# Optimization experiments

Hardware: AMD Instinct MI355X
Metric: run time of the kernel (lower is better)

## Reference

```python
import jax, jax.numpy as jnp
import numpy as np

B, T, D_MODEL, D_HIDDEN, MAX_SEQLEN = 4, 2048, 1024, 256, 2048


def setup_inputs() -> dict:
    key = jax.random.key(0)
    ks = jax.random.split(key, 8)
    s_in = 1.0 / np.sqrt(D_MODEL)
    s_out = 1.0 / np.sqrt(D_HIDDEN)
    # xavier_uniform bound for W_bias (fan_in = fan_out = MAX_SEQLEN)
    xb = np.sqrt(6.0 / (MAX_SEQLEN + MAX_SEQLEN))
    return {
        "q": jax.random.normal(ks[0], (B, T, D_MODEL), jnp.float32),
        "k": jax.random.normal(ks[1], (B, T, D_MODEL), jnp.float32),
        "v": jax.random.normal(ks[2], (B, T, D_MODEL), jnp.float32),
        "Wq": jax.random.normal(ks[3], (D_MODEL, D_HIDDEN), jnp.float32) * s_in,
        "Wk": jax.random.normal(ks[4], (D_MODEL, D_HIDDEN), jnp.float32) * s_in,
        "Wv": jax.random.normal(ks[5], (D_MODEL, D_HIDDEN), jnp.float32) * s_in,
        "Wo": jax.random.normal(ks[6], (D_HIDDEN, D_MODEL), jnp.float32) * s_out,
        "W_bias": jax.random.uniform(ks[7], (MAX_SEQLEN, MAX_SEQLEN), jnp.float32, -xb, xb),
    }


def reference(q, k, v, Wq, Wk, Wv, Wo, W_bias):
    Ti, Tj = q.shape[1], k.shape[1]
    Q = q @ Wq                      # [B,Ti,dh]
    K = k @ Wk                      # [B,Tj,dh]
    V = v @ Wv                      # [B,Tj,dh]
    pos_bias = W_bias[:Ti, :Tj][None]               # [1,Ti,Tj]
    # NOTE: source subtracts max over dim 0 (batch). For pos_bias that dim is 1,
    # so exp_pos_bias == exp(0) == ones -- reproduced faithfully here.
    max_key = jnp.max(K, axis=0, keepdims=True)      # [1,Tj,dh]
    max_pos_bias = jnp.max(pos_bias, axis=0, keepdims=True)
    exp_key = jnp.exp(K - max_key)                   # [B,Tj,dh]
    exp_pos_bias = jnp.exp(pos_bias - max_pos_bias)  # [1,Ti,Tj]
    num = jnp.einsum('ij,bjd->bid', exp_pos_bias[0], exp_key * V)  # [B,Ti,dh]
    den = jnp.einsum('ij,bjd->bid', exp_pos_bias[0], exp_key)      # [B,Ti,dh]
    Yt = jax.nn.sigmoid(Q) * num / den
    return Yt @ Wo                  # [B,Ti,d_model]
```

## Files before the change

kernel.cpp:

```cpp
#include <hip/hip_runtime.h>
#include <hip/hip_bf16.h>
#include <math.h>

#define B_   4
#define T_   2048
#define DM   1024
#define DH   256
#define M_   (B_*T_)

typedef __bf16 bf16;
typedef __attribute__((ext_vector_type(8))) __bf16 bf16x8;
typedef __attribute__((ext_vector_type(4))) float  f32x4;

__device__ inline float sigmoidf_(float x) { return 1.0f / (1.0f + __expf(-x)); }

__device__ inline int swz8(int r, int c) { return (((c >> 3) ^ (r & 7)) << 3); }

__global__ void transpose_cvt_all(const float* __restrict__ Wq, const float* __restrict__ Wk,
                                  const float* __restrict__ Wv, const float* __restrict__ Wo,
                                  bf16* __restrict__ Wq_t, bf16* __restrict__ Wk_t,
                                  bf16* __restrict__ Wv_t, bf16* __restrict__ Wo_t)
{
    const int bid = blockIdx.x;
    __shared__ float tile[32][33];
    const int w = bid >> 8, t = bid & 255;
    const float* in; bf16* out; int R, C, sh;
    if      (w == 0) { in = Wq; out = Wq_t; R = DM; C = DH; sh = 3; }
    else if (w == 1) { in = Wk; out = Wk_t; R = DM; C = DH; sh = 3; }
    else if (w == 2) { in = Wv; out = Wv_t; R = DM; C = DH; sh = 3; }
    else             { in = Wo; out = Wo_t; R = DH; C = DM; sh = 5; }
    const int r0 = (t >> sh) * 32, c0 = (t & ((1 << sh) - 1)) * 32;
    const int tx = threadIdx.x & 31, ty = threadIdx.x >> 5;
    #pragma unroll
    for (int i = ty; i < 32; i += 8)
        tile[i][tx] = in[(long)(r0 + i) * C + c0 + tx];
    __syncthreads();
    #pragma unroll
    for (int i = ty; i < 32; i += 8)
        out[(long)(c0 + i) * R + r0 + tx] = (bf16)tile[tx][i];
}

__global__ __launch_bounds__(512, 6)
void gemm_proj(const float* __restrict__ qin, const float* __restrict__ kin,
               const float* __restrict__ vin,
               const bf16* __restrict__ Wq_t, const bf16* __restrict__ Wk_t,
               const bf16* __restrict__ Wv_t,
               bf16* __restrict__ Yb, bf16* __restrict__ Kb, bf16* __restrict__ Vb)
{
    __shared__ __align__(16) bf16 As[2][64][64];
    __shared__ __align__(16) bf16 Bs[2][128][64];

    const int z = blockIdx.z;
    const float* A  = (z == 0) ? qin  : (z == 1) ? kin  : vin;
    const bf16*  Wt = (z == 0) ? Wq_t : (z == 1) ? Wk_t : Wv_t;
    bf16*        C  = (z == 0) ? Yb   : (z == 1) ? Kb   : Vb;

    const int bid  = blockIdx.x;
    const int tile = (bid & 7) * 32 + (bid >> 3);
    const int m0 = (tile >> 1) * 64;
    const int n0 = (tile & 1) * 128;

    const int tid = threadIdx.x, lane = tid & 63, wave = tid >> 6;
    const int wr = wave >> 2, wc = wave & 3;
    const int q4 = lane >> 4, l16 = lane & 15;

    f32x4 acc[2][2] = {};
    const int ar = tid >> 3, ac8 = (tid & 7) * 8;
    const int br = tid >> 2, bc16 = (tid & 3) * 16;

    const float* aBase = &A[(long)(m0 + ar) * DM + ac8];
    const bf16*  bBase = &Wt[(long)(n0 + br) * DM + bc16];

    f32x4  pa0[2], pa1[2];
    bf16x8 pb0[2], pb1[2];
    #pragma unroll
    for (int p = 0; p < 2; ++p) {
        const float* ap = aBase + p * 64;
        pa0[p] = *(const f32x4*)ap; pa1[p] = *(const f32x4*)(ap + 4);
        const bf16* bp = bBase + p * 64;
        pb0[p] = *(const bf16x8*)bp; pb1[p] = *(const bf16x8*)(bp + 8);
    }
    {
        bf16x8 o;
        #pragma unroll
        for (int e = 0; e < 4; ++e) { o[e] = (bf16)pa0[0][e]; o[4 + e] = (bf16)pa1[0][e]; }
        *(bf16x8*)&As[0][ar][swz8(ar, ac8)]      = o;
        *(bf16x8*)&Bs[0][br][swz8(br, bc16)]     = pb0[0];
        *(bf16x8*)&Bs[0][br][swz8(br, bc16 + 8)] = pb1[0];
    }
    __syncthreads();

    #pragma unroll
    for (int s = 0; s < 16; ++s) {
        const int cs = s & 1;
        const int ns = cs ^ 1;
        if (s + 2 < 16) {
            const float* ap = aBase + (s + 2) * 64;
            pa0[cs] = *(const f32x4*)ap; pa1[cs] = *(const f32x4*)(ap + 4);
            const bf16* bp = bBase + (s + 2) * 64;
            pb0[cs] = *(const bf16x8*)bp; pb1[cs] = *(const bf16x8*)(bp + 8);
        }
        if (s + 1 < 16) {
            bf16x8 o;
            #pragma unroll
            for (int e = 0; e < 4; ++e) { o[e] = (bf16)pa0[ns][e]; o[4 + e] = (bf16)pa1[ns][e]; }
            *(bf16x8*)&As[ns][ar][swz8(ar, ac8)]      = o;
            *(bf16x8*)&Bs[ns][br][swz8(br, bc16)]     = pb0[ns];
            *(bf16x8*)&Bs[ns][br][swz8(br, bc16 + 8)] = pb1[ns];
        }
        #pragma unroll
        for (int kk = 0; kk < 64; kk += 32) {
            const int ra = wr * 32 + l16, rb = wc * 32 + l16;
            bf16x8 a0 = *(const bf16x8*)&As[cs][ra     ][swz8(ra,      kk + q4 * 8)];
            bf16x8 a1 = *(const bf16x8*)&As[cs][ra + 16][swz8(ra + 16, kk + q4 * 8)];
            bf16x8 b0 = *(const bf16x8*)&Bs[cs][rb     ][swz8(rb,      kk + q4 * 8)];
            bf16x8 b1 = *(const bf16x8*)&Bs[cs][rb + 16][swz8(rb + 16, kk + q4 * 8)];
            acc[0][0] = __builtin_amdgcn_mfma_f32_16x16x32_bf16(a0, b0, acc[0][0], 0, 0, 0);
            acc[0][1] = __builtin_amdgcn_mfma_f32_16x16x32_bf16(a0, b1, acc[0][1], 0, 0, 0);
            acc[1][0] = __builtin_amdgcn_mfma_f32_16x16x32_bf16(a1, b0, acc[1][0], 0, 0, 0);
            acc[1][1] = __builtin_amdgcn_mfma_f32_16x16x32_bf16(a1, b1, acc[1][1], 0, 0, 0);
        }
        __syncthreads();
    }
    #pragma unroll
    for (int i = 0; i < 2; ++i)
        #pragma unroll
        for (int j = 0; j < 2; ++j)
            #pragma unroll
            for (int r = 0; r < 4; ++r) {
                int gm = m0 + wr * 32 + i * 16 + q4 * 4 + r;
                int gn = n0 + wc * 32 + j * 16 + l16;
                float v = acc[i][j][r];
                C[(long)gm * DH + gn] = (bf16)((z == 0) ? sigmoidf_(v) : v);
            }
}

__global__ void reduce_kv(const bf16* __restrict__ Kb, const bf16* __restrict__ Vb,
                          float* __restrict__ part)
{
    __shared__ float red[2][4][B_][DH];
    const int tid = threadIdx.x;
    const int g = tid & 31, jj = tid >> 5;
    const int d8 = g * 8;

    float sn[B_][8] = {}, sd[B_][8] = {};
    #pragma unroll
    for (int t2 = 0; t2 < 2; ++t2) {
        const int j = blockIdx.x * 16 + t2 * 8 + jj;
        bf16x8 kx[B_], vx[B_];
        #pragma unroll
        for (int b = 0; b < B_; ++b) {
            kx[b] = *(const bf16x8*)&Kb[((long)b * T_ + j) * DH + d8];
            vx[b] = *(const bf16x8*)&Vb[((long)b * T_ + j) * DH + d8];
        }
        #pragma unroll
        for (int e = 0; e < 8; ++e) {
            float k0 = (float)kx[0][e], k1 = (float)kx[1][e];
            float k2 = (float)kx[2][e], k3 = (float)kx[3][e];
            float mx = fmaxf(fmaxf(k0, k1), fmaxf(k2, k3));
            float e0 = __expf(k0 - mx), e1 = __expf(k1 - mx);
            float e2 = __expf(k2 - mx), e3 = __expf(k3 - mx);
            sn[0][e] += e0 * (float)vx[0][e]; sd[0][e] += e0;
            sn[1][e] += e1 * (float)vx[1][e]; sd[1][e] += e1;
            sn[2][e] += e2 * (float)vx[2][e]; sd[2][e] += e2;
            sn[3][e] += e3 * (float)vx[3][e]; sd[3][e] += e3;
        }
    }
    #pragma unroll
    for (int b = 0; b < B_; ++b)
        #pragma unroll
        for (int e = 0; e < 8; ++e) {
            sn[b][e] += __shfl_xor(sn[b][e], 32);
            sd[b][e] += __shfl_xor(sd[b][e], 32);
        }
    const int w = tid >> 6;
    if ((tid & 32) == 0) {
        #pragma unroll
        for (int b = 0; b < B_; ++b)
            #pragma unroll
            for (int e = 0; e < 8; ++e) {
                red[0][w][b][d8 + e] = sn[b][e];
                red[1][w][b][d8 + e] = sd[b][e];
            }
    }
    __syncthreads();
    float* pout = &part[(long)blockIdx.x * 2048];
    #pragma unroll
    for (int o = tid; o < 2 * B_ * DH; o += 256) {
        const int arr = o >> 10, b = (o >> 8) & 3, d = o & 255;
        pout[o] = red[arr][0][b][d] + red[arr][1][b][d]
                + red[arr][2][b][d] + red[arr][3][b][d];
    }
}

__global__ void merge_kv(const float* __restrict__ part, float* __restrict__ rv)
{
    const int t = blockIdx.x * 256 + threadIdx.x;
    float num = 0.f, den = 0.f;
    for (int blk = 0; blk < 128; ++blk) {
        num += part[(long)blk * 2048 + t];
        den += part[(long)blk * 2048 + 1024 + t];
    }
    rv[t] = num / den;
}

__global__ __launch_bounds__(512, 6)
void gemm_out(const bf16* __restrict__ Yb, const bf16* __restrict__ Wo_t,
              const float* __restrict__ rv, float* __restrict__ out)
{
    __shared__ __align__(16) bf16 As[2][64][64];
    __shared__ __align__(16) bf16 Bs[2][128][64];
    __shared__ float rv_s[DH];

    const int bid  = blockIdx.x;
    const int tile = (bid & 7) * 128 + (bid >> 3);
    const int m0 = (tile >> 3) * 64;
    const int n0 = (tile & 7) * 128;
    const int b  = m0 >> 11;

    const int tid = threadIdx.x, lane = tid & 63, wave = tid >> 6;
    const int wr = wave >> 2, wc = wave & 3;
    const int q4 = lane >> 4, l16 = lane & 15;

    if (tid < DH) rv_s[tid] = rv[b * DH + tid];

    f32x4 acc[2][2] = {};
    const int ar = tid >> 3, ac8 = (tid & 7) * 8;
    const int br = tid >> 2, bc16 = (tid & 3) * 16;

    const bf16* aBase = &Yb[(long)(m0 + ar) * DH + ac8];
    const bf16* bBase = &Wo_t[(long)(n0 + br) * DH + bc16];

    bf16x8 pq[2], pb0[2], pb1[2];
    #pragma unroll
    for (int p = 0; p < 2; ++p) {
        pq[p]  = *(const bf16x8*)(aBase + p * 64);
        const bf16* wp = bBase + p * 64;
        pb0[p] = *(const bf16x8*)wp; pb1[p] = *(const bf16x8*)(wp + 8);
    }
    __syncthreads();
    {
        bf16x8 o;
        #pragma unroll
        for (int e = 0; e < 8; ++e)
            o[e] = (bf16)((float)pq[0][e] * rv_s[ac8 + e]);
        *(bf16x8*)&As[0][ar][swz8(ar, ac8)]      = o;
        *(bf16x8*)&Bs[0][br][swz8(br, bc16)]     = pb0[0];
        *(bf16x8*)&Bs[0][br][swz8(br, bc16 + 8)] = pb1[0];
    }
    __syncthreads();

    #pragma unroll
    for (int s = 0; s < 4; ++s) {
        const int cs = s & 1, ns = cs ^ 1;
        if (s + 2 < 4) {
            pq[cs]  = *(const bf16x8*)(aBase + (s + 2) * 64);
            const bf16* wp = bBase + (s + 2) * 64;
            pb0[cs] = *(const bf16x8*)wp; pb1[cs] = *(const bf16x8*)(wp + 8);
        }
        if (s + 1 < 4) {
            bf16x8 o;
            #pragma unroll
            for (int e = 0; e < 8; ++e)
                o[e] = (bf16)((float)pq[ns][e] * rv_s[(s + 1) * 64 + ac8 + e]);
            *(bf16x8*)&As[ns][ar][swz8(ar, ac8)]      = o;
            *(bf16x8*)&Bs[ns][br][swz8(br, bc16)]     = pb0[ns];
            *(bf16x8*)&Bs[ns][br][swz8(br, bc16 + 8)] = pb1[ns];
        }
        #pragma unroll
        for (int kk = 0; kk < 64; kk += 32) {
            const int ra = wr * 32 + l16, rb = wc * 32 + l16;
            bf16x8 a0 = *(const bf16x8*)&As[cs][ra     ][swz8(ra,      kk + q4 * 8)];
            bf16x8 a1 = *(const bf16x8*)&As[cs][ra + 16][swz8(ra + 16, kk + q4 * 8)];
            bf16x8 b0 = *(const bf16x8*)&Bs[cs][rb     ][swz8(rb,      kk + q4 * 8)];
            bf16x8 b1 = *(const bf16x8*)&Bs[cs][rb + 16][swz8(rb + 16, kk + q4 * 8)];
            acc[0][0] = __builtin_amdgcn_mfma_f32_16x16x32_bf16(a0, b0, acc[0][0], 0, 0, 0);
            acc[0][1] = __builtin_amdgcn_mfma_f32_16x16x32_bf16(a0, b1, acc[0][1], 0, 0, 0);
            acc[1][0] = __builtin_amdgcn_mfma_f32_16x16x32_bf16(a1, b0, acc[1][0], 0, 0, 0);
            acc[1][1] = __builtin_amdgcn_mfma_f32_16x16x32_bf16(a1, b1, acc[1][1], 0, 0, 0);
        }
        __syncthreads();
    }
    #pragma unroll
    for (int i = 0; i < 2; ++i)
        #pragma unroll
        for (int j = 0; j < 2; ++j)
            #pragma unroll
            for (int r = 0; r < 4; ++r) {
                int gm = m0 + wr * 32 + i * 16 + q4 * 4 + r;
                int gn = n0 + wc * 32 + j * 16 + l16;
                out[(long)gm * DM + gn] = acc[i][j][r];
            }
}

extern "C" void kernel_launch(void* const* d_in, const int* in_sizes, int n_in,
                              void* d_out, int out_size, void* d_ws, size_t ws_size,
                              hipStream_t stream)
{
    const float* q  = (const float*)d_in[0];
    const float* k  = (const float*)d_in[1];
    const float* v  = (const float*)d_in[2];
    const float* Wq = (const float*)d_in[3];
    const float* Wk = (const float*)d_in[4];
    const float* Wv = (const float*)d_in[5];
    const float* Wo = (const float*)d_in[6];
    float* out = (float*)d_out;

    char* ws = (char*)d_ws;
    bf16* Yb    = (bf16*)ws;  ws += (size_t)M_ * DH * sizeof(bf16);
    bf16* Kb    = (bf16*)ws;  ws += (size_t)M_ * DH * sizeof(bf16);
    bf16* Vb    = (bf16*)ws;  ws += (size_t)M_ * DH * sizeof(bf16);
    bf16* Wq_t  = (bf16*)ws;  ws += (size_t)DM * DH * sizeof(bf16);
    bf16* Wk_t  = (bf16*)ws;  ws += (size_t)DM * DH * sizeof(bf16);
    bf16* Wv_t  = (bf16*)ws;  ws += (size_t)DM * DH * sizeof(bf16);
    bf16* Wo_t  = (bf16*)ws;  ws += (size_t)DM * DH * sizeof(bf16);
    float* rv   = (float*)ws; ws += (size_t)B_ * DH * sizeof(float);
    float* part = (float*)ws; ws += (size_t)128 * 2048 * sizeof(float);

    transpose_cvt_all<<<1024, 256, 0, stream>>>(Wq, Wk, Wv, Wo,
                                                Wq_t, Wk_t, Wv_t, Wo_t);

    gemm_proj<<<dim3(256, 1, 3), 512, 0, stream>>>(q, k, v, Wq_t, Wk_t, Wv_t,
                                                   Yb, Kb, Vb);
    reduce_kv<<<128, 256, 0, stream>>>(Kb, Vb, part);
    merge_kv<<<4, 256, 0, stream>>>(part, rv);
    gemm_out<<<1024, 512, 0, stream>>>(Yb, Wo_t, rv, out);
}
```

Measured before the change: 199.4 us.

## Fuse K/V projection with exp-weighted reduction into one kernel

The K and V projection GEMMs now run in the same block, with rows arranged so each tile holds the same 16 time positions across all 4 batches. The batch-max softmax and the num/den partial sums are then computed in shared memory straight from the accumulators. This removes the Kb/Vb bf16 round trip through global memory and the separate reduce_kv launch. In exchange, K/V blocks do twice the GEMM work serially, so the grid becomes unbalanced: z=1 blocks take about twice as long as the Q blocks.

```diff
diff --git a/kernel.cpp b/kernel.cpp
--- a/kernel.cpp
+++ b/kernel.cpp
@@ -40,50 +40,206 @@
         out[(long)(c0 + i) * R + r0 + tx] = (bf16)tile[tx][i];
 }
 
+#define GEMM_PHASE(APTR, WT, ACC) {                                           \
+    const float* aBase = &(APTR)[arowg * DM + ac8];                           \
+    const bf16*  bBase = &(WT)[(long)(n0 + br) * DM + bc16];                  \
+    f32x4 pa0[2], pa1[2]; bf16x8 pb0[2], pb1[2];                              \
+    _Pragma("unroll")                                                         \
+    for (int p = 0; p < 2; ++p) {                                             \
+        const float* ap = aBase + p * 64;                                     \
+        pa0[p] = *(const f32x4*)ap; pa1[p] = *(const f32x4*)(ap + 4);         \
+        const bf16* bp = bBase + p * 64;                                      \
+        pb0[p] = *(const bf16x8*)bp; pb1[p] = *(const bf16x8*)(bp + 8);       \
+    }                                                                         \
+    {   bf16x8 o;                                                             \
+        _Pragma("unroll")                                                     \
+        for (int e = 0; e < 4; ++e) { o[e] = (bf16)pa0[0][e]; o[4+e] = (bf16)pa1[0][e]; } \
+        *(bf16x8*)&As[0][ar][swz8(ar, ac8)]      = o;                         \
+        *(bf16x8*)&Bs[0][br][swz8(br, bc16)]     = pb0[0];                    \
+        *(bf16x8*)&Bs[0][br][swz8(br, bc16 + 8)] = pb1[0];                    \
+    }                                                                         \
+    __syncthreads();                                                          \
+    _Pragma("unroll")                                                         \
+    for (int s = 0; s < 16; ++s) {                                            \
+        const int cs = s & 1, ns = cs ^ 1;                                    \
+        if (s + 2 < 16) {                                                     \
+            const float* ap = aBase + (s + 2) * 64;                           \
+            pa0[cs] = *(const f32x4*)ap; pa1[cs] = *(const f32x4*)(ap + 4);   \
+            const bf16* bp = bBase + (s + 2) * 64;                            \
+            pb0[cs] = *(const bf16x8*)bp; pb1[cs] = *(const bf16x8*)(bp + 8); \
+        }                                                                     \
+        if (s + 1 < 16) {                                                     \
+            bf16x8 o;                                                         \
+            _Pragma("unroll")                                                 \
+            for (int e = 0; e < 4; ++e) { o[e] = (bf16)pa0[ns][e]; o[4+e] = (bf16)pa1[ns][e]; } \
+            *(bf16x8*)&As[ns][ar][swz8(ar, ac8)]      = o;                    \
+            *(bf16x8*)&Bs[ns][br][swz8(br, bc16)]     = pb0[ns];              \
+            *(bf16x8*)&Bs[ns][br][swz8(br, bc16 + 8)] = pb1[ns];              \
+        }                                                                     \
+        _Pragma("unroll")                                                     \
+        for (int kk = 0; kk < 64; kk += 32) {                                 \
+            const int ra = wr * 32 + l16, rb = wc * 32 + l16;                 \
+            bf16x8 a0 = *(const bf16x8*)&As[cs][ra     ][swz8(ra,      kk + q4 * 8)]; \
+            bf16x8 a1 = *(const bf16x8*)&As[cs][ra + 16][swz8(ra + 16, kk + q4 * 8)]; \
+            bf16x8 b0 = *(const bf16x8*)&Bs[cs][rb     ][swz8(rb,      kk + q4 * 8)]; \
+            bf16x8 b1 = *(const bf16x8*)&Bs[cs][rb + 16][swz8(rb + 16, kk + q4 * 8)]; \
+            ACC[0][0] = __builtin_amdgcn_mfma_f32_16x16x32_bf16(a0, b0, ACC[0][0], 0, 0, 0); \
+            ACC[0][1] = __builtin_amdgcn_mfma_f32_16x16x32_bf16(a0, b1, ACC[0][1], 0, 0, 0); \
+            ACC[1][0] = __builtin_amdgcn_mfma_f32_16x16x32_bf16(a1, b0, ACC[1][0], 0, 0, 0); \
+            ACC[1][1] = __builtin_amdgcn_mfma_f32_16x16x32_bf16(a1, b1, ACC[1][1], 0, 0, 0); \
+        }                                                                     \
+        __syncthreads();                                                      \
+    } }
+
 __global__ __launch_bounds__(512, 6)
-void gemm_proj(const float* __restrict__ qin, const float* __restrict__ kin,
-               const float* __restrict__ vin,
-               const bf16* __restrict__ Wq_t, const bf16* __restrict__ Wk_t,
-               const bf16* __restrict__ Wv_t,
-               bf16* __restrict__ Yb, bf16* __restrict__ Kb, bf16* __restrict__ Vb)
-{
-    __shared__ __align__(16) bf16 As[2][64][64];
-    __shared__ __align__(16) bf16 Bs[2][128][64];
-
-    const int z = blockIdx.z;
-    const float* A  = (z == 0) ? qin  : (z == 1) ? kin  : vin;
-    const bf16*  Wt = (z == 0) ? Wq_t : (z == 1) ? Wk_t : Wv_t;
-    bf16*        C  = (z == 0) ? Yb   : (z == 1) ? Kb   : Vb;
-
-    const int bid  = blockIdx.x;
+void proj_fused(const float* __restrict__ qin, const float* __restrict__ kin,
+                const float* __restrict__ vin,
+                const bf16* __restrict__ Wq_t, const bf16* __restrict__ Wk_t,
+                const bf16* __restrict__ Wv_t,
+                bf16* __restrict__ Yb, float* __restrict__ part_num,
+                float* __restrict__ part_den)
+{
+    __shared__ __align__(16) char smem[49152];
+    auto As = reinterpret_cast<bf16 (*)[64][64]>(smem);
+    auto Bs = reinterpret_cast<bf16 (*)[128][64]>(smem + 16384);
+
+    const int z   = blockIdx.z;
+    const int bid = blockIdx.x;
     const int tile = (bid & 7) * 32 + (bid >> 3);
-    const int m0 = (tile >> 1) * 64;
     const int n0 = (tile & 1) * 128;
 
     const int tid = threadIdx.x, lane = tid & 63, wave = tid >> 6;
     const int wr = wave >> 2, wc = wave & 3;
     const int q4 = lane >> 4, l16 = lane & 15;
+    const int ar = tid >> 3, ac8 = (tid & 7) * 8;
+    const int br = tid >> 2, bc16 = (tid & 3) * 16;
+
+    const int m0 = (tile >> 1) * 64;
+    const int jt = tile >> 1;
+    const long arowg = (z == 0) ? (long)(m0 + ar)
+                                : (long)(ar >> 4) * T_ + jt * 16 + (ar & 15);
+
+    f32x4 accA[2][2] = {};
+    f32x4 accV[2][2] = {};
+
+    if (z == 0) {
+        GEMM_PHASE(qin, Wq_t, accA)
+        #pragma unroll
+        for (int i = 0; i < 2; ++i)
+            #pragma unroll
+            for (int j = 0; j < 2; ++j)
+                #pragma unroll
+                for (int r = 0; r < 4; ++r) {
+                    int gm = m0 + wr * 32 + i * 16 + q4 * 4 + r;
+                    int gn = n0 + wc * 32 + j * 16 + l16;
+                    Yb[(long)gm * DH + gn] = (bf16)sigmoidf_(accA[i][j][r]);
+                }
+    } else {
+        GEMM_PHASE(kin, Wk_t, accA)
+        GEMM_PHASE(vin, Wv_t, accV)
+        auto KL = reinterpret_cast<bf16 (*)[128]>(smem);
+        auto VL = reinterpret_cast<bf16 (*)[128]>(smem + 16384);
+        float* red_n = (float*)(smem + 32768);
+        float* red_d = (float*)(smem + 40960);
+        #pragma unroll
+        for (int i = 0; i < 2; ++i)
+            #pragma unroll
+            for (int j = 0; j < 2; ++j)
+                #pragma unroll
+                for (int r = 0; r < 4; ++r) {
+                    const int row = wr * 32 + i * 16 + q4 * 4 + r;
+                    const int col = wc * 32 + j * 16 + l16;
+                    KL[row][col] = (bf16)accA[i][j][r];
+                    VL[row][col] = (bf16)accV[i][j][r];
+                }
+        __syncthreads();
+        const int d = tid & 127, grp = tid >> 7;
+        float sn0 = 0.f, sn1 = 0.f, sn2 = 0.f, sn3 = 0.f;
+        float sd0 = 0.f, sd1 = 0.f, sd2 = 0.f, sd3 = 0.f;
+        #pragma unroll
+        for (int jj4 = 0; jj4 < 4; ++jj4) {
+            const int jjj = grp * 4 + jj4;
+            float k0 = (float)KL[jjj][d],      k1 = (float)KL[16 + jjj][d];
+            float k2 = (float)KL[32 + jjj][d], k3 = (float)KL[48 + jjj][d];
+            float mx = fmaxf(fmaxf(k0, k1), fmaxf(k2, k3));
+            float e0 = __expf(k0 - mx), e1 = __expf(k1 - mx);
+            float e2 = __expf(k2 - mx), e3 = __expf(k3 - mx);
+            sn0 += e0 * (float)VL[jjj][d];      sd0 += e0;
+            sn1 += e1 * (float)VL[16 + jjj][d]; sd1 += e1;
+            sn2 += e2 * (float)VL[32 + jjj][d]; sd2 += e2;
+            sn3 += e3 * (float)VL[48 + jjj][d]; sd3 += e3;
+        }
+        red_n[(grp * 4 + 0) * 128 + d] = sn0; red_d[(grp * 4 + 0) * 128 + d] = sd0;
+        red_n[(grp * 4 + 1) * 128 + d] = sn1; red_d[(grp * 4 + 1) * 128 + d] = sd1;
+        red_n[(grp * 4 + 2) * 128 + d] = sn2; red_d[(grp * 4 + 2) * 128 + d] = sd2;
+        red_n[(grp * 4 + 3) * 128 + d] = sn3; red_d[(grp * 4 + 3) * 128 + d] = sd3;
+        __syncthreads();
+        {
+            const int b = tid >> 7, dd = tid & 127;
+            float num = red_n[(b) * 128 + dd]      + red_n[(4 + b) * 128 + dd]
+                      + red_n[(8 + b) * 128 + dd]  + red_n[(12 + b) * 128 + dd];
+            float den = red_d[(b) * 128 + dd]      + red_d[(4 + b) * 128 + dd]
+                      + red_d[(8 + b) * 128 + dd]  + red_d[(12 + b) * 128 + dd];
+            const int idx = ((jt * 4 + b) << 8) + n0 + dd;
+            part_num[idx] = num;
+            part_den[idx] = den;
+        }
+    }
+}
+
+__global__ void merge_kv(const float* __restrict__ pn, const float* __restrict__ pd,
+                         float* __restrict__ rv)
+{
+    const int t = blockIdx.x * 256 + threadIdx.x;
+    const int b = t >> 8, d = t & 255;
+    float num = 0.f, den = 0.f;
+    for (int jt = 0; jt < 128; ++jt) {
+        num += pn[((jt * 4 + b) << 8) + d];
+        den += pd[((jt * 4 + b) << 8) + d];
+    }
+    rv[t] = num / den;
+}
+
+__global__ __launch_bounds__(512, 6)
+void gemm_out(const bf16* __restrict__ Yb, const bf16* __restrict__ Wo_t,
+              const float* __restrict__ rv, float* __restrict__ out)
+{
+    __shared__ __align__(16) bf16 As[2][64][64];
+    __shared__ __align__(16) bf16 Bs[2][128][64];
+    __shared__ float rv_s[DH];
+
+    const int bid  = blockIdx.x;
+    const int tile = (bid & 7) * 128 + (bid >> 3);
+    const int m0 = (tile >> 3) * 64;
+    const int n0 = (tile & 7) * 128;
+    const int b  = m0 >> 11;
+
+    const int tid = threadIdx.x, lane = tid & 63, wave = tid >> 6;
+    const int wr = wave >> 2, wc = wave & 3;
+    const int q4 = lane >> 4, l16 = lane & 15;
+
+    if (tid < DH) rv_s[tid] = rv[b * DH + tid];
 
     f32x4 acc[2][2] = {};
     const int ar = tid >> 3, ac8 = (tid & 7) * 8;
     const int br = tid >> 2, bc16 = (tid & 3) * 16;
 
-    const float* aBase = &A[(long)(m0 + ar) * DM + ac8];
-    const bf16*  bBase = &Wt[(long)(n0 + br) * DM + bc16];
-
-    f32x4  pa0[2], pa1[2];
-    bf16x8 pb0[2], pb1[2];
+    const bf16* aBase = &Yb[(long)(m0 + ar) * DH + ac8];
+    const bf16* bBase = &Wo_t[(long)(n0 + br) * DH + bc16];
+
+    bf16x8 pq[2], pb0[2], pb1[2];
     #pragma unroll
     for (int p = 0; p < 2; ++p) {
-        const float* ap = aBase + p * 64;
-        pa0[p] = *(const f32x4*)ap; pa1[p] = *(const f32x4*)(ap + 4);
-        const bf16* bp = bBase + p * 64;
-        pb0[p] = *(const bf16x8*)bp; pb1[p] = *(const bf16x8*)(bp + 8);
-    }
+        pq[p]  = *(const bf16x8*)(aBase + p * 64);
+        const bf16* wp = bBase + p * 64;
+        pb0[p] = *(const bf16x8*)wp; pb1[p] = *(const bf16x8*)(wp + 8);
+    }
+    __syncthreads();
     {
         bf16x8 o;
         #pragma unroll
-        for (int e = 0; e < 4; ++e) { o[e] = (bf16)pa0[0][e]; o[4 + e] = (bf16)pa1[0][e]; }
+        for (int e = 0; e < 8; ++e)
+            o[e] = (bf16)((float)pq[0][e] * rv_s[ac8 + e]);
         *(bf16x8*)&As[0][ar][swz8(ar, ac8)]      = o;
         *(bf16x8*)&Bs[0][br][swz8(br, bc16)]     = pb0[0];
         *(bf16x8*)&Bs[0][br][swz8(br, bc16 + 8)] = pb1[0];
@@ -91,19 +247,18 @@
     __syncthreads();
 
     #pragma unroll
-    for (int s = 0; s < 16; ++s) {
-        const int cs = s & 1;
-        const int ns = cs ^ 1;
-        if (s + 2 < 16) {
-            const float* ap = aBase + (s + 2) * 64;
-            pa0[cs] = *(const f32x4*)ap; pa1[cs] = *(const f32x4*)(ap + 4);
-            const bf16* bp = bBase + (s + 2) * 64;
-            pb0[cs] = *(const bf16x8*)bp; pb1[cs] = *(const bf16x8*)(bp + 8);
-        }
-        if (s + 1 < 16) {
+    for (int s = 0; s < 4; ++s) {
+        const int cs = s & 1, ns = cs ^ 1;
+        if (s + 2 < 4) {
+            pq[cs]  = *(const bf16x8*)(aBase + (s + 2) * 64);
+            const bf16* wp = bBase + (s + 2) * 64;
+            pb0[cs] = *(const bf16x8*)wp; pb1[cs] = *(const bf16x8*)(wp + 8);
+        }
+        if (s + 1 < 4) {
             bf16x8 o;
             #pragma unroll
-            for (int e = 0; e < 4; ++e) { o[e] = (bf16)pa0[ns][e]; o[4 + e] = (bf16)pa1[ns][e]; }
+            for (int e = 0; e < 8; ++e)
+                o[e] = (bf16)((float)pq[ns][e] * rv_s[(s + 1) * 64 + ac8 + e]);
             *(bf16x8*)&As[ns][ar][swz8(ar, ac8)]      = o;
             *(bf16x8*)&Bs[ns][br][swz8(br, bc16)]     = pb0[ns];
             *(bf16x8*)&Bs[ns][br][swz8(br, bc16 + 8)] = pb1[ns];
@@ -130,165 +285,6 @@
             for (int r = 0; r < 4; ++r) {
                 int gm = m0 + wr * 32 + i * 16 + q4 * 4 + r;
                 int gn = n0 + wc * 32 + j * 16 + l16;
-                float v = acc[i][j][r];
-                C[(long)gm * DH + gn] = (bf16)((z == 0) ? sigmoidf_(v) : v);
-            }
-}
-
-__global__ void reduce_kv(const bf16* __restrict__ Kb, const bf16* __restrict__ Vb,
-                          float* __restrict__ part)
-{
-    __shared__ float red[2][4][B_][DH];
-    const int tid = threadIdx.x;
-    const int g = tid & 31, jj = tid >> 5;
-    const int d8 = g * 8;
-
-    float sn[B_][8] = {}, sd[B_][8] = {};
-    #pragma unroll
-    for (int t2 = 0; t2 < 2; ++t2) {
-        const int j = blockIdx.x * 16 + t2 * 8 + jj;
-        bf16x8 kx[B_], vx[B_];
-        #pragma unroll
-        for (int b = 0; b < B_; ++b) {
-            kx[b] = *(const bf16x8*)&Kb[((long)b * T_ + j) * DH + d8];
-            vx[b] = *(const bf16x8*)&Vb[((long)b * T_ + j) * DH + d8];
-        }
-        #pragma unroll
-        for (int e = 0; e < 8; ++e) {
-            float k0 = (float)kx[0][e], k1 = (float)kx[1][e];
-            float k2 = (float)kx[2][e], k3 = (float)kx[3][e];
-            float mx = fmaxf(fmaxf(k0, k1), fmaxf(k2, k3));
-            float e0 = __expf(k0 - mx), e1 = __expf(k1 - mx);
-            float e2 = __expf(k2 - mx), e3 = __expf(k3 - mx);
-            sn[0][e] += e0 * (float)vx[0][e]; sd[0][e] += e0;
-            sn[1][e] += e1 * (float)vx[1][e]; sd[1][e] += e1;
-            sn[2][e] += e2 * (float)vx[2][e]; sd[2][e] += e2;
-            sn[3][e] += e3 * (float)vx[3][e]; sd[3][e] += e3;
-        }
-    }
-    #pragma unroll
-    for (int b = 0; b < B_; ++b)
-        #pragma unroll
-        for (int e = 0; e < 8; ++e) {
-            sn[b][e] += __shfl_xor(sn[b][e], 32);
-            sd[b][e] += __shfl_xor(sd[b][e], 32);
-        }
-    const int w = tid >> 6;
-    if ((tid & 32) == 0) {
-        #pragma unroll
-        for (int b = 0; b < B_; ++b)
-            #pragma unroll
-            for (int e = 0; e < 8; ++e) {
-                red[0][w][b][d8 + e] = sn[b][e];
-                red[1][w][b][d8 + e] = sd[b][e];
-            }
-    }
-    __syncthreads();
-    float* pout = &part[(long)blockIdx.x * 2048];
-    #pragma unroll
-    for (int o = tid; o < 2 * B_ * DH; o += 256) {
-        const int arr = o >> 10, b = (o >> 8) & 3, d = o & 255;
-        pout[o] = red[arr][0][b][d] + red[arr][1][b][d]
-                + red[arr][2][b][d] + red[arr][3][b][d];
-    }
-}
-
-__global__ void merge_kv(const float* __restrict__ part, float* __restrict__ rv)
-{
-    const int t = blockIdx.x * 256 + threadIdx.x;
-    float num = 0.f, den = 0.f;
-    for (int blk = 0; blk < 128; ++blk) {
-        num += part[(long)blk * 2048 + t];
-        den += part[(long)blk * 2048 + 1024 + t];
-    }
-    rv[t] = num / den;
-}
-
-__global__ __launch_bounds__(512, 6)
-void gemm_out(const bf16* __restrict__ Yb, const bf16* __restrict__ Wo_t,
-              const float* __restrict__ rv, float* __restrict__ out)
-{
-    __shared__ __align__(16) bf16 As[2][64][64];
-    __shared__ __align__(16) bf16 Bs[2][128][64];
-    __shared__ float rv_s[DH];
-
-    const int bid  = blockIdx.x;
-    const int tile = (bid & 7) * 128 + (bid >> 3);
-    const int m0 = (tile >> 3) * 64;
-    const int n0 = (tile & 7) * 128;
-    const int b  = m0 >> 11;
-
-    const int tid = threadIdx.x, lane = tid & 63, wave = tid >> 6;
-    const int wr = wave >> 2, wc = wave & 3;
-    const int q4 = lane >> 4, l16 = lane & 15;
-
-    if (tid < DH) rv_s[tid] = rv[b * DH + tid];
-
-    f32x4 acc[2][2] = {};
-    const int ar = tid >> 3, ac8 = (tid & 7) * 8;
-    const int br = tid >> 2, bc16 = (tid & 3) * 16;
-
-    const bf16* aBase = &Yb[(long)(m0 + ar) * DH + ac8];
-    const bf16* bBase = &Wo_t[(long)(n0 + br) * DH + bc16];
-
-    bf16x8 pq[2], pb0[2], pb1[2];
-    #pragma unroll
-    for (int p = 0; p < 2; ++p) {
-        pq[p]  = *(const bf16x8*)(aBase + p * 64);
-        const bf16* wp = bBase + p * 64;
-        pb0[p] = *(const bf16x8*)wp; pb1[p] = *(const bf16x8*)(wp + 8);
-    }
-    __syncthreads();
-    {
-        bf16x8 o;
-        #pragma unroll
-        for (int e = 0; e < 8; ++e)
-            o[e] = (bf16)((float)pq[0][e] * rv_s[ac8 + e]);
-        *(bf16x8*)&As[0][ar][swz8(ar, ac8)]      = o;
-        *(bf16x8*)&Bs[0][br][swz8(br, bc16)]     = pb0[0];
-        *(bf16x8*)&Bs[0][br][swz8(br, bc16 + 8)] = pb1[0];
-    }
-    __syncthreads();
-
-    #pragma unroll
-    for (int s = 0; s < 4; ++s) {
-        const int cs = s & 1, ns = cs ^ 1;
-        if (s + 2 < 4) {
-            pq[cs]  = *(const bf16x8*)(aBase + (s + 2) * 64);
-            const bf16* wp = bBase + (s + 2) * 64;
-            pb0[cs] = *(const bf16x8*)wp; pb1[cs] = *(const bf16x8*)(wp + 8);
-        }
-        if (s + 1 < 4) {
-            bf16x8 o;
-            #pragma unroll
-            for (int e = 0; e < 8; ++e)
-                o[e] = (bf16)((float)pq[ns][e] * rv_s[(s + 1) * 64 + ac8 + e]);
-            *(bf16x8*)&As[ns][ar][swz8(ar, ac8)]      = o;
-            *(bf16x8*)&Bs[ns][br][swz8(br, bc16)]     = pb0[ns];
-            *(bf16x8*)&Bs[ns][br][swz8(br, bc16 + 8)] = pb1[ns];
-        }
-        #pragma unroll
-        for (int kk = 0; kk < 64; kk += 32) {
-            const int ra = wr * 32 + l16, rb = wc * 32 + l16;
-            bf16x8 a0 = *(const bf16x8*)&As[cs][ra     ][swz8(ra,      kk + q4 * 8)];
-            bf16x8 a1 = *(const bf16x8*)&As[cs][ra + 16][swz8(ra + 16, kk + q4 * 8)];
-            bf16x8 b0 = *(const bf16x8*)&Bs[cs][rb     ][swz8(rb,      kk + q4 * 8)];
-            bf16x8 b1 = *(const bf16x8*)&Bs[cs][rb + 16][swz8(rb + 16, kk + q4 * 8)];
-            acc[0][0] = __builtin_amdgcn_mfma_f32_16x16x32_bf16(a0, b0, acc[0][0], 0, 0, 0);
-            acc[0][1] = __builtin_amdgcn_mfma_f32_16x16x32_bf16(a0, b1, acc[0][1], 0, 0, 0);
-            acc[1][0] = __builtin_amdgcn_mfma_f32_16x16x32_bf16(a1, b0, acc[1][0], 0, 0, 0);
-            acc[1][1] = __builtin_amdgcn_mfma_f32_16x16x32_bf16(a1, b1, acc[1][1], 0, 0, 0);
-        }
-        __syncthreads();
-    }
-    #pragma unroll
-    for (int i = 0; i < 2; ++i)
-        #pragma unroll
-        for (int j = 0; j < 2; ++j)
-            #pragma unroll
-            for (int r = 0; r < 4; ++r) {
-                int gm = m0 + wr * 32 + i * 16 + q4 * 4 + r;
-                int gn = n0 + wc * 32 + j * 16 + l16;
                 out[(long)gm * DM + gn] = acc[i][j][r];
             }
 }
@@ -307,22 +303,20 @@
     float* out = (float*)d_out;
 
     char* ws = (char*)d_ws;
-    bf16* Yb    = (bf16*)ws;  ws += (size_t)M_ * DH * sizeof(bf16);
-    bf16* Kb    = (bf16*)ws;  ws += (size_t)M_ * DH * sizeof(bf16);
-    bf16* Vb    = (bf16*)ws;  ws += (size_t)M_ * DH * sizeof(bf16);
-    bf16* Wq_t  = (bf16*)ws;  ws += (size_t)DM * DH * sizeof(bf16);
-    bf16* Wk_t  = (bf16*)ws;  ws += (size_t)DM * DH * sizeof(bf16);
-    bf16* Wv_t  = (bf16*)ws;  ws += (size_t)DM * DH * sizeof(bf16);
-    bf16* Wo_t  = (bf16*)ws;  ws += (size_t)DM * DH * sizeof(bf16);
-    float* rv   = (float*)ws; ws += (size_t)B_ * DH * sizeof(float);
-    float* part = (float*)ws; ws += (size_t)128 * 2048 * sizeof(float);
+    bf16* Yb       = (bf16*)ws;  ws += (size_t)M_ * DH * sizeof(bf16);
+    bf16* Wq_t     = (bf16*)ws;  ws += (size_t)DM * DH * sizeof(bf16);
+    bf16* Wk_t     = (bf16*)ws;  ws += (size_t)DM * DH * sizeof(bf16);
+    bf16* Wv_t     = (bf16*)ws;  ws += (size_t)DM * DH * sizeof(bf16);
+    bf16* Wo_t     = (bf16*)ws;  ws += (size_t)DM * DH * sizeof(bf16);
+    float* rv      = (float*)ws; ws += (size_t)B_ * DH * sizeof(float);
+    float* part_n  = (float*)ws; ws += (size_t)128 * 4 * 256 * sizeof(float);
+    float* part_d  = (float*)ws; ws += (size_t)128 * 4 * 256 * sizeof(float);
 
     transpose_cvt_all<<<1024, 256, 0, stream>>>(Wq, Wk, Wv, Wo,
                                                 Wq_t, Wk_t, Wv_t, Wo_t);
 
-    gemm_proj<<<dim3(256, 1, 3), 512, 0, stream>>>(q, k, v, Wq_t, Wk_t, Wv_t,
-                                                   Yb, Kb, Vb);
-    reduce_kv<<<128, 256, 0, stream>>>(Kb, Vb, part);
-    merge_kv<<<4, 256, 0, stream>>>(part, rv);
+    proj_fused<<<dim3(256, 1, 2), 512, 0, stream>>>(q, k, v, Wq_t, Wk_t, Wv_t,
+                                                    Yb, part_n, part_d);
+    merge_kv<<<4, 256, 0, stream>>>(part_n, part_d, rv);
     gemm_out<<<1024, 512, 0, stream>>>(Yb, Wo_t, rv, out);
 }
```

Measured after the change: 195.9 us. No clear change (-1.8%).
